# Optimization experiments

Hardware: AMD Instinct MI355X
Metric: run time of the kernel (lower is better)

The kernel has to match this reference:

```python
import jax, jax.numpy as jnp
import numpy as np

TEMPERATURE = 0.07
UNIFORMITY_THRESHOLD = 0.1
SEPARATION_MARGIN = 2.0
W_SUPCON = 1.0
W_SEPARATION = 0.5
W_UNIFORMITY = 0.5
NUM_MASKS = 6


def setup_inputs() -> dict:
    key = jax.random.key(0)
    k1, k2, k3 = jax.random.split(key, 3)
    B, H, Wd, D = 16, 33, 33, 512
    emb = jax.random.normal(k1, (B, H, Wd, D), dtype=jnp.float32)
    emb = emb / jnp.linalg.norm(emb, axis=-1, keepdims=True)  # module expects normalized embeddings
    masks = jax.random.uniform(k2, (B, NUM_MASKS, H, Wd), dtype=jnp.float32)
    is_forged = jax.random.uniform(k3, (B,), dtype=jnp.float32)
    return {"embeddings": emb, "masks": masks, "is_forged": is_forged}


def _labels(masks):
    # masks: (M, H, W). Channel i writes label i+1 where mask>0.5 (if channel has any mass);
    # later channels overwrite earlier -> equivalent to max over active hits.
    active = masks.sum(axis=(1, 2)) > 0  # (M,)
    hit = (masks > 0.5) & active[:, None, None]
    ids = jnp.arange(1, masks.shape[0] + 1)[:, None, None]
    return jnp.max(jnp.where(hit, ids, 0), axis=0).reshape(-1)  # (H*W,)


def _per_image(emb, masks, forged):
    H, W, D = emb.shape
    feat = emb.reshape(-1, D)  # (N, D)
    N = feat.shape[0]
    labels = _labels(masks)  # (N,) in 0..M
    L = masks.shape[0] + 1  # possible labels 0..6
    onehot = (labels[:, None] == jnp.arange(L)[None, :]).astype(feat.dtype)  # (N, L)
    cnt = onehot.sum(axis=0)  # (L,)
    sums = onehot.T @ feat  # (L, D) per-label sums
    mean_l = sums / jnp.maximum(cnt, 1.0)[:, None]  # safe per-label centroids

    # ---- SupCon (PixelSupConLoss) ----
    logits = (feat @ feat.T) / TEMPERATURE  # (N, N)
    logits = logits - jax.lax.stop_gradient(logits.max(axis=1, keepdims=True))
    same = (labels[:, None] == labels[None, :]).astype(feat.dtype)
    logits_mask = 1.0 - jnp.eye(N, dtype=feat.dtype)
    pos = same * logits_mask
    exp_l = jnp.exp(logits) * logits_mask
    log_prob = logits - jnp.log(exp_l.sum(axis=1, keepdims=True) + 1e-6)
    pos_sum = pos.sum(axis=1)
    mean_lp = (pos * log_prob).sum(axis=1) / jnp.where(pos_sum == 0, 1.0, pos_sum)
    anchor_valid = (pos_sum > 0).astype(feat.dtype)
    n_anchor = anchor_valid.sum()
    supcon = (-mean_lp * anchor_valid).sum() / jnp.maximum(n_anchor, 1.0)
    supcon_valid = n_anchor > 0

    # ---- Inter-instance separation ----
    present = cnt > 0
    cn = (mean_l ** 2).sum(axis=1)  # (L,)
    sq = cn[:, None] + cn[None, :] - 2.0 * (mean_l @ mean_l.T)  # squared centroid dists
    tri = jnp.triu(jnp.ones((L, L), dtype=bool), k=1)
    pair_valid = tri & present[:, None] & present[None, :]
    d = jnp.sqrt(jnp.where(pair_valid, jnp.maximum(sq, 0.0), 1.0))
    terms = jnp.where(pair_valid, jax.nn.relu(SEPARATION_MARGIN - d), 0.0)
    n_pairs = pair_valid.sum().astype(feat.dtype)
    sep = terms.sum() / jnp.maximum(n_pairs, 1.0)
    sep_valid = present.sum() >= 2

    # ---- Uniformity ----
    rn2 = (feat ** 2).sum(axis=1)  # (N,)
    q_l = onehot.T @ rn2  # (L,) per-label sum of squared norms
    var_l = q_l / jnp.maximum(cnt, 1.0) - (mean_l ** 2).sum(axis=1)  # E||e||^2 - ||mean||^2
    lbl_valid = (cnt >= 2) & (var_l > UNIFORMITY_THRESHOLD)
    inst_loss = jnp.where(lbl_valid, var_l - UNIFORMITY_THRESHOLD, 0.0).sum()
    n_lbl = lbl_valid.sum().astype(feat.dtype)
    uni_forged = inst_loss / jnp.maximum(n_lbl, 1.0)
    uni_forged_valid = n_lbl > 0
    mean_all = feat.mean(axis=0)
    var_all = ((feat - mean_all) ** 2).sum(axis=1).mean()
    uni_unf = jnp.where(var_all > UNIFORMITY_THRESHOLD, var_all - UNIFORMITY_THRESHOLD, 0.0)
    uni_unf_valid = var_all > UNIFORMITY_THRESHOLD

    is_f = forged >= 0.5
    uni = jnp.where(is_f, uni_forged, uni_unf)
    uni_valid = jnp.where(is_f, uni_forged_valid, uni_unf_valid)
    return supcon, supcon_valid, sep, sep_valid, uni, uni_valid


def _agg(vals, valids):
    v = valids.astype(vals.dtype)
    n = v.sum()
    return jnp.where(n > 0, (vals * v).sum() / jnp.maximum(n, 1.0), 0.0)


def reference(embeddings, masks, is_forged):
    sc, scv, sp, spv, un, unv = jax.vmap(_per_image)(embeddings, masks, is_forged)
    supcon = _agg(sc, scv)
    separation = _agg(sp, spv)
    uniformity = _agg(un, unv)
    return W_SUPCON * supcon + W_SEPARATION * separation + W_UNIFORMITY * uniformity
```

## Files before the change

### kernel.cpp

```cpp
#include <hip/hip_runtime.h>
#include <math.h>

#define NPIX 1089
#define DIM 512
#define NIMG 16
#define NLBL 8
#define NMASK 6
#define INVT 14.2857142857142857f

#define NGRP 72
#define NROWPAD 1152
#define NT9 9


typedef short v8s __attribute__((ext_vector_type(8)));
typedef float v4f __attribute__((ext_vector_type(4)));

__device__ __forceinline__ float wave_reduce(float x) {
#pragma unroll
  for (int o = 32; o > 0; o >>= 1) x += __shfl_xor(x, o, 64);
  return x;
}
__device__ __forceinline__ unsigned bfbits(float x) {
  unsigned u = __float_as_uint(x);
  return (u + 0x7FFFu + ((u >> 16) & 1u)) >> 16;
}
__device__ __forceinline__ unsigned pk(float lo, float hi) {
  return bfbits(lo) | (bfbits(hi) << 16);
}

__global__ __launch_bounds__(512) void k_packsum(const float* __restrict__ emb,
                                                 const float* __restrict__ masks,
                                                 uint2* __restrict__ bfemb2,
                                                 float* __restrict__ sums9,
                                                 unsigned* __restrict__ counter) {
  int b = blockIdx.y;
  int g9 = blockIdx.x >> 1, dh = blockIdx.x & 1;
  int tid = threadIdx.x, dd = tid & 63, w4 = tid >> 6, lane = tid & 63;
  __shared__ float msum[NMASK];
  __shared__ int slab[128];
  __shared__ float4 red[8 * 8 * 64];
  if (tid < NMASK) msum[tid] = 0.f;
  if (tid == 0 && blockIdx.x == 0 && b == 0) *counter = 0u;
  __syncthreads();
  {
    float am[NMASK] = {0.f, 0.f, 0.f, 0.f, 0.f, 0.f};
    for (int p = tid; p < NPIX; p += 512) {
#pragma unroll
      for (int c = 0; c < NMASK; c++) am[c] += masks[((size_t)b * NMASK + c) * NPIX + p];
    }
#pragma unroll
    for (int c = 0; c < NMASK; c++) {
      float v = wave_reduce(am[c]);
      if (lane == 0) atomicAdd(&msum[c], v);
    }
  }
  __syncthreads();
  if (tid < 128) {
    int r = g9 * 128 + tid;
    int lab = 7;
    if (r < NPIX) {
      lab = 0;
#pragma unroll
      for (int c = 0; c < NMASK; c++) {
        float mv = masks[((size_t)b * NMASK + c) * NPIX + r];
        if (mv > 0.5f && msum[c] > 0.f) lab = c + 1;
      }
    }
    slab[tid] = lab;
  }
  __syncthreads();
  float4 fa0 = {0,0,0,0}, fa1 = {0,0,0,0}, fa2 = {0,0,0,0}, fa3 = {0,0,0,0};
  float4 fa4 = {0,0,0,0}, fa5 = {0,0,0,0}, fa6 = {0,0,0,0}, fa7 = {0,0,0,0};
  int kc = dh * 8 + (dd >> 3), q = (dd >> 1) & 3, half = dd & 1;
#pragma unroll
  for (int k = 0; k < 16; k++) {
    int r = g9 * 128 + w4 + k * 8;
    bool v = r < NPIX;
    int rc = v ? r : (NPIX - 1);
    float4 x = ((const float4*)(emb + (size_t)(b * NPIX + rc) * DIM))[dh * 64 + dd];
    if (!v) x = make_float4(0.f, 0.f, 0.f, 0.f);
    uint2 o = make_uint2(pk(x.x, x.y), pk(x.z, x.w));
    bfemb2[((((size_t)(b * NGRP + (r >> 4)) * 16 + kc) * 64) + q * 16 + (r & 15)) * 2 + half] = o;
    int lab = __builtin_amdgcn_readfirstlane(slab[r - g9 * 128]);
    switch (lab) {
      case 0: fa0.x += x.x; fa0.y += x.y; fa0.z += x.z; fa0.w += x.w; break;
      case 1: fa1.x += x.x; fa1.y += x.y; fa1.z += x.z; fa1.w += x.w; break;
      case 2: fa2.x += x.x; fa2.y += x.y; fa2.z += x.z; fa2.w += x.w; break;
      case 3: fa3.x += x.x; fa3.y += x.y; fa3.z += x.z; fa3.w += x.w; break;
      case 4: fa4.x += x.x; fa4.y += x.y; fa4.z += x.z; fa4.w += x.w; break;
      case 5: fa5.x += x.x; fa5.y += x.y; fa5.z += x.z; fa5.w += x.w; break;
      case 6: fa6.x += x.x; fa6.y += x.y; fa6.z += x.z; fa6.w += x.w; break;
      default: fa7.x += x.x; fa7.y += x.y; fa7.z += x.z; fa7.w += x.w; break;
    }
  }
  red[(0 * 8 + w4) * 64 + dd] = fa0; red[(1 * 8 + w4) * 64 + dd] = fa1;
  red[(2 * 8 + w4) * 64 + dd] = fa2; red[(3 * 8 + w4) * 64 + dd] = fa3;
  red[(4 * 8 + w4) * 64 + dd] = fa4; red[(5 * 8 + w4) * 64 + dd] = fa5;
  red[(6 * 8 + w4) * 64 + dd] = fa6; red[(7 * 8 + w4) * 64 + dd] = fa7;
  __syncthreads();
  int l = tid >> 6, d2 = tid & 63;
  float4 s = {0,0,0,0};
#pragma unroll
  for (int ww = 0; ww < 8; ww++) {
    float4 t = red[(l * 8 + ww) * 64 + d2];
    s.x += t.x; s.y += t.y; s.z += t.z; s.w += t.w;
  }
  *(float4*)&sums9[(((size_t)(b * NT9 + g9) * NLBL + l) * DIM) + dh * 256 + d2 * 4] = s;
}

__global__ __launch_bounds__(256) void k_epass3(const uint4* __restrict__ bfemb4,
                                                float* __restrict__ E9) {
  int n = blockIdx.x;
  int img = ((n & 7) << 1) | ((n >> 3) & 1);
  int t = n >> 4;
  int it = 0, rem = t;
  while (rem >= NT9 - it) { rem -= NT9 - it; it++; }
  int jt = it + rem;
  int i0 = it * 128, j0 = jt * 128;
  bool diag = (it == jt);
  int tid = threadIdx.x, lane = tid & 63, w = tid >> 6;
  int wm = w >> 1, wn = w & 1;
  int quad = lane >> 4, l15 = lane & 15;
  __shared__ float Ered[2][128];
  __shared__ float Ecol[2][128];

  size_t uA[4], uB[4];
#pragma unroll
  for (int f = 0; f < 4; f++) {
    uA[f] = ((size_t)(img * NGRP + it * 8 + wm * 4 + f) * 16) * 64 + lane;
    uB[f] = ((size_t)(img * NGRP + jt * 8 + wn * 4 + f) * 16) * 64 + lane;
  }

  v4f acc[4][4];
#pragma unroll
  for (int mf = 0; mf < 4; mf++)
#pragma unroll
    for (int nf = 0; nf < 4; nf++) acc[mf][nf] = (v4f){0.f, 0.f, 0.f, 0.f};

  v8s a0[4], b0[4], a1[4], b1[4];
#define LOADG(kc, AR, BR)                                               \
  {                                                                     \
    _Pragma("unroll") for (int f = 0; f < 4; f++)                       \
        AR[f] = *(const v8s*)(bfemb4 + uA[f] + (kc) * 64);              \
    _Pragma("unroll") for (int f = 0; f < 4; f++)                       \
        BR[f] = *(const v8s*)(bfemb4 + uB[f] + (kc) * 64);              \
  }
#define MFMAG(AR, BR)                                                   \
  {                                                                     \
    _Pragma("unroll") for (int mf = 0; mf < 4; mf++)                    \
        _Pragma("unroll") for (int nf = 0; nf < 4; nf++)                \
            acc[mf][nf] = __builtin_amdgcn_mfma_f32_16x16x32_bf16(      \
                AR[mf], BR[nf], acc[mf][nf], 0, 0, 0);                  \
  }

  LOADG(0, a0, b0);
#pragma unroll
  for (int kc = 0; kc < 16; kc += 2) {
    if (kc + 1 < 16) LOADG(kc + 1, a1, b1);
    MFMAG(a0, b0);
    if (kc + 2 < 16) LOADG(kc + 2, a0, b0);
    MFMAG(a1, b1);
  }
#undef LOADG
#undef MFMAG

  float scol[4] = {0.f, 0.f, 0.f, 0.f};
#pragma unroll
  for (int mf = 0; mf < 4; mf++) {
#pragma unroll
    for (int rr = 0; rr < 4; rr++) {
      int i = i0 + wm * 64 + mf * 16 + quad * 4 + rr;
      float srow = 0.f;
#pragma unroll
      for (int nf = 0; nf < 4; nf++) {
        int j = j0 + wn * 64 + nf * 16 + l15;
        float e = __expf((acc[mf][nf][rr] - 1.f) * INVT);
        bool ok = (j < NPIX) && (!diag || (i != j && i < NPIX));
        e = ok ? e : 0.f;
        srow += e;
        scol[nf] += e;
      }
      srow += __shfl_xor(srow, 1); srow += __shfl_xor(srow, 2);
      srow += __shfl_xor(srow, 4); srow += __shfl_xor(srow, 8);
      if (l15 == 0) Ered[wn][wm * 64 + mf * 16 + quad * 4 + rr] = srow;
    }
  }
  if (!diag) {
#pragma unroll
    for (int nf = 0; nf < 4; nf++) {
      float s = scol[nf];
      s += __shfl_xor(s, 16); s += __shfl_xor(s, 32);
      if (quad == 0) Ecol[wm][wn * 64 + nf * 16 + l15] = s;
    }
  }
  __syncthreads();
  if (tid < 128) {
    E9[((size_t)img * NT9 + jt) * NROWPAD + i0 + tid] = Ered[0][tid] + Ered[1][tid];
    if (!diag)
      E9[((size_t)img * NT9 + it) * NROWPAD + j0 + tid] = Ecol[0][tid] + Ecol[1][tid];
  }
}

__global__ void k_imgfinal(const float* __restrict__ masks, const float* __restrict__ sums9,
                           const float* __restrict__ E9, const float* __restrict__ is_forged,
                           unsigned* __restrict__ counter, float* __restrict__ per_img,
                           float* __restrict__ out) {
  int b = blockIdx.x, tid = threadIdx.x;
  int wave = tid >> 6, lane = tid & 63;
  __shared__ float msum[NMASK];
  __shared__ int slab[NPIX];
  __shared__ float ssum[NLBL * DIM];
  __shared__ float sCnt[NLBL], sR[NLBL][NLBL];
  __shared__ float red4[4][NLBL];
  __shared__ float sLog, sNA;
  if (tid < NMASK) msum[tid] = 0.f;
  if (tid == 0) { sLog = 0.f; sNA = 0.f; }
  __syncthreads();
  {
    float am[NMASK] = {0.f, 0.f, 0.f, 0.f, 0.f, 0.f};
    for (int p = tid; p < NPIX; p += 256) {
#pragma unroll
      for (int c = 0; c < NMASK; c++) am[c] += masks[((size_t)b * NMASK + c) * NPIX + p];
    }
#pragma unroll
    for (int c = 0; c < NMASK; c++) {
      float v = wave_reduce(am[c]);
      if (lane == 0) atomicAdd(&msum[c], v);
    }
  }
  __syncthreads();
  {
    float c8[NLBL] = {0.f, 0.f, 0.f, 0.f, 0.f, 0.f, 0.f, 0.f};
    for (int p = tid; p < NPIX; p += 256) {
      int lab = 0;
#pragma unroll
      for (int c = 0; c < NMASK; c++) {
        float mv = masks[((size_t)b * NMASK + c) * NPIX + p];
        if (mv > 0.5f && msum[c] > 0.f) lab = c + 1;
      }
      slab[p] = lab;
#pragma unroll
      for (int l = 0; l < NLBL; l++) c8[l] += (lab == l) ? 1.f : 0.f;
    }
#pragma unroll
    for (int l = 0; l < NLBL; l++) c8[l] = wave_reduce(c8[l]);
    if (lane == 0) {
#pragma unroll
      for (int l = 0; l < NLBL; l++) red4[wave][l] = c8[l];
    }
  }
  __syncthreads();
  if (tid < NLBL)
    sCnt[tid] = red4[0][tid] + red4[1][tid] + red4[2][tid] + red4[3][tid];
  for (int o = tid; o < NLBL * DIM; o += 256) {
    float s = 0.f;
#pragma unroll
    for (int g = 0; g < NT9; g++) s += sums9[((size_t)(b * NT9 + g) * NLBL * DIM) + o];
    ssum[o] = s;
  }
  __syncthreads();
  float ll = 0.f, na = 0.f;
  for (int p = tid; p < NPIX; p += 256) {
    int lab = slab[p];
    if (sCnt[lab] >= 1.5f) {
      float e = 0.f;
#pragma unroll
      for (int s = 0; s < NT9; s++) e += E9[((size_t)b * NT9 + s) * NROWPAD + p];
      ll += logf(e + 1e-6f);
      na += 1.f;
    }
  }
  ll = wave_reduce(ll); na = wave_reduce(na);
  if (lane == 0) { atomicAdd(&sLog, ll); atomicAdd(&sNA, na); }
  for (int t = wave; t < 36; t += 4) {
    int a = 0, tt = t;
    while (tt >= NLBL - a) { tt -= NLBL - a; a++; }
    int bb = a + tt;
    float d0 = 0.f;
    for (int k = lane; k < DIM; k += 64) d0 += ssum[a * DIM + k] * ssum[bb * DIM + k];
    d0 = wave_reduce(d0);
    if (lane == 0) sR[a][bb] = d0;
  }
  __syncthreads();
  if (tid == 0) {
    float spos = 0.f;
    for (int l = 0; l < NLBL; l++) {
      float c = sCnt[l];
      if (c >= 1.5f) spos += (sR[l][l] - c) * INVT / (c - 1.f) - c * INVT;
    }
    float nA = sNA;
    float sc = nA > 0.f ? (sLog - spos) / nA : 0.f;
    float scv = nA > 0.f ? 1.f : 0.f;
    float inv[NLBL]; int present[NLBL]; int nPres = 0;
    for (int l = 0; l < NLBL; l++) {
      present[l] = sCnt[l] > 0.f;
      nPres += present[l];
      inv[l] = 1.f / fmaxf(sCnt[l], 1.f);
    }
    float sepsum = 0.f; int npairs = 0;
    for (int a = 0; a < NLBL; a++)
      for (int c = a + 1; c < NLBL; c++)
        if (present[a] && present[c]) {
          float sq_ = sR[a][a] * inv[a] * inv[a] + sR[c][c] * inv[c] * inv[c]
                    - 2.f * sR[a][c] * inv[a] * inv[c];
          float dd = sqrtf(fmaxf(sq_, 0.f));
          sepsum += fmaxf(2.f - dd, 0.f);
          npairs++;
        }
    float sep = npairs > 0 ? sepsum / (float)npairs : 0.f;
    float sepv = nPres >= 2 ? 1.f : 0.f;
    float inst = 0.f; int nlbl = 0;
    for (int l = 0; l < NLBL; l++) {
      float var = 1.f - sR[l][l] * inv[l] * inv[l];
      if (sCnt[l] >= 2.f && var > 0.1f) { inst += var - 0.1f; nlbl++; }
    }
    float unif = nlbl > 0 ? inst / (float)nlbl : 0.f;
    float unifv = nlbl > 0 ? 1.f : 0.f;
    float tot2 = 0.f;
    for (int a = 0; a < NLBL; a++) {
      tot2 += sR[a][a];
      for (int c = a + 1; c < NLBL; c++) tot2 += 2.f * sR[a][c];
    }
    float Nf = (float)NPIX;
    float var_all = 1.f - tot2 / (Nf * Nf);
    float uniu = var_all > 0.1f ? var_all - 0.1f : 0.f;
    float uniuv = var_all > 0.1f ? 1.f : 0.f;
    bool isf = is_forged[b] >= 0.5f;
    per_img[b * 6 + 0] = sc;
    per_img[b * 6 + 1] = scv;
    per_img[b * 6 + 2] = sep;
    per_img[b * 6 + 3] = sepv;
    per_img[b * 6 + 4] = isf ? unif : uniu;
    per_img[b * 6 + 5] = isf ? unifv : uniuv;
    __threadfence();
    unsigned tk = atomicAdd(counter, 1u);
    if (tk == NIMG - 1) {
      __threadfence();
      float accv[3] = {0.f, 0.f, 0.f}, accn[3] = {0.f, 0.f, 0.f};
      for (int bb = 0; bb < NIMG; bb++)
        for (int m = 0; m < 3; m++) {
          float v = per_img[bb * 6 + m * 2], val = per_img[bb * 6 + m * 2 + 1];
          accv[m] += v * val; accn[m] += val;
        }
      float scA = accn[0] > 0.f ? accv[0] / accn[0] : 0.f;
      float sepA = accn[1] > 0.f ? accv[1] / accn[1] : 0.f;
      float uniA = accn[2] > 0.f ? accv[2] / accn[2] : 0.f;
      out[0] = 1.0f * scA + 0.5f * sepA + 0.5f * uniA;
    }
  }
}

extern "C" void kernel_launch(void* const* d_in, const int* in_sizes, int n_in,
                              void* d_out, int out_size, void* d_ws, size_t ws_size,
                              hipStream_t stream) {
  const float* emb = (const float*)d_in[0];
  const float* masks = (const float*)d_in[1];
  const float* isf = (const float*)d_in[2];
  float* out = (float*)d_out;
  char* ws = (char*)d_ws;
  size_t off = 0;
  uint4* bfemb4 = (uint4*)(ws + off);
  off += (size_t)NIMG * NGRP * 16 * 64 * 16;
  float* E9 = (float*)(ws + off);     off += sizeof(float) * NIMG * NT9 * NROWPAD;
  float* sums9 = (float*)(ws + off);  off += sizeof(float) * NIMG * NT9 * NLBL * DIM;
  float* per_img = (float*)(ws + off); off += sizeof(float) * NIMG * 6;
  off = (off + 127) & ~(size_t)127;
  unsigned* counter = (unsigned*)(ws + off); off += 128;

  k_packsum<<<dim3(18, NIMG), 512, 0, stream>>>(emb, masks, (uint2*)bfemb4, sums9, counter);
  k_epass3<<<45 * NIMG, 256, 0, stream>>>(bfemb4, E9);
  k_imgfinal<<<NIMG, 256, 0, stream>>>(masks, sums9, E9, isf, counter, per_img, out);
}
```

Before: 142.7 us.

## Fuse per-image final reduction into GEMM kernel via last-block tail

Removes the separate per-image final kernel. The last of the 45 tile blocks for each image, detected with a per-image atomic counter, now does the final reduction itself. Labels and per-chunk label counts are precomputed in the pack kernel, so the tail no longer re-reads the masks or recomputes labels. This saves one kernel launch and its serialization gap. In exchange, the GEMM kernel carries roughly 18KB of extra shared memory for the tail, which may lower occupancy, and it switches log to the faster __logf.

Result: slower. 174.8 us (+22.5%).

```diff
diff --git a/kernel.cpp b/kernel.cpp
--- a/kernel.cpp
+++ b/kernel.cpp
@@ -33,15 +33,19 @@
                                                  const float* __restrict__ masks,
                                                  uint2* __restrict__ bfemb2,
                                                  float* __restrict__ sums9,
-                                                 unsigned* __restrict__ counter) {
+                                                 int* __restrict__ labels,
+                                                 float* __restrict__ cnt9,
+                                                 unsigned* __restrict__ counters) {
   int b = blockIdx.y;
   int g9 = blockIdx.x >> 1, dh = blockIdx.x & 1;
   int tid = threadIdx.x, dd = tid & 63, w4 = tid >> 6, lane = tid & 63;
   __shared__ float msum[NMASK];
   __shared__ int slab[128];
+  __shared__ int scnt[NLBL];
   __shared__ float4 red[8 * 8 * 64];
   if (tid < NMASK) msum[tid] = 0.f;
-  if (tid == 0 && blockIdx.x == 0 && b == 0) *counter = 0u;
+  if (tid < NLBL) scnt[tid] = 0;
+  if (b == 0 && blockIdx.x == 0 && tid < 17) counters[tid] = 0u;
   __syncthreads();
   {
     float am[NMASK] = {0.f, 0.f, 0.f, 0.f, 0.f, 0.f};
@@ -68,8 +72,13 @@
       }
     }
     slab[tid] = lab;
-  }
-  __syncthreads();
+    if (dh == 0) {
+      labels[b * NROWPAD + r] = lab;
+      if (r < NPIX) atomicAdd(&scnt[lab], 1);
+    }
+  }
+  __syncthreads();
+  if (dh == 0 && tid < NLBL) cnt9[((size_t)b * NT9 + g9) * NLBL + tid] = (float)scnt[tid];
   float4 fa0 = {0,0,0,0}, fa1 = {0,0,0,0}, fa2 = {0,0,0,0}, fa3 = {0,0,0,0};
   float4 fa4 = {0,0,0,0}, fa5 = {0,0,0,0}, fa6 = {0,0,0,0}, fa7 = {0,0,0,0};
   int kc = dh * 8 + (dd >> 3), q = (dd >> 1) & 3, half = dd & 1;
@@ -109,8 +118,15 @@
   *(float4*)&sums9[(((size_t)(b * NT9 + g9) * NLBL + l) * DIM) + dh * 256 + d2 * 4] = s;
 }
 
-__global__ __launch_bounds__(256) void k_epass3(const uint4* __restrict__ bfemb4,
-                                                float* __restrict__ E9) {
+__global__ __launch_bounds__(256) void k_epass4(const uint4* __restrict__ bfemb4,
+                                                const float* __restrict__ sums9,
+                                                const int* __restrict__ labels,
+                                                const float* __restrict__ cnt9,
+                                                const float* __restrict__ is_forged,
+                                                unsigned* __restrict__ counters,
+                                                float* __restrict__ E9,
+                                                float* __restrict__ per_img,
+                                                float* __restrict__ out) {
   int n = blockIdx.x;
   int img = ((n & 7) << 1) | ((n >> 3) & 1);
   int t = n >> 4;
@@ -124,6 +140,11 @@
   int quad = lane >> 4, l15 = lane & 15;
   __shared__ float Ered[2][128];
   __shared__ float Ecol[2][128];
+  __shared__ int slab[NPIX];
+  __shared__ float ssum[NLBL * DIM];
+  __shared__ float sCnt[NLBL], sR[NLBL][NLBL];
+  __shared__ float sLog, sNA;
+  __shared__ int isTail;
 
   size_t uA[4], uB[4];
 #pragma unroll
@@ -200,63 +221,25 @@
     if (!diag)
       E9[((size_t)img * NT9 + it) * NROWPAD + j0 + tid] = Ecol[0][tid] + Ecol[1][tid];
   }
-}
-
-__global__ void k_imgfinal(const float* __restrict__ masks, const float* __restrict__ sums9,
-                           const float* __restrict__ E9, const float* __restrict__ is_forged,
-                           unsigned* __restrict__ counter, float* __restrict__ per_img,
-                           float* __restrict__ out) {
-  int b = blockIdx.x, tid = threadIdx.x;
-  int wave = tid >> 6, lane = tid & 63;
-  __shared__ float msum[NMASK];
-  __shared__ int slab[NPIX];
-  __shared__ float ssum[NLBL * DIM];
-  __shared__ float sCnt[NLBL], sR[NLBL][NLBL];
-  __shared__ float red4[4][NLBL];
-  __shared__ float sLog, sNA;
-  if (tid < NMASK) msum[tid] = 0.f;
+  __threadfence();
+  __syncthreads();
+  if (tid == 0) isTail = (atomicAdd(&counters[img], 1u) == 44u);
+  __syncthreads();
+  if (!isTail) return;
+  __threadfence();
+
+  if (tid < NLBL) {
+    float s = 0.f;
+#pragma unroll
+    for (int g = 0; g < NT9; g++) s += cnt9[((size_t)img * NT9 + g) * NLBL + tid];
+    sCnt[tid] = s;
+  }
   if (tid == 0) { sLog = 0.f; sNA = 0.f; }
-  __syncthreads();
-  {
-    float am[NMASK] = {0.f, 0.f, 0.f, 0.f, 0.f, 0.f};
-    for (int p = tid; p < NPIX; p += 256) {
-#pragma unroll
-      for (int c = 0; c < NMASK; c++) am[c] += masks[((size_t)b * NMASK + c) * NPIX + p];
-    }
-#pragma unroll
-    for (int c = 0; c < NMASK; c++) {
-      float v = wave_reduce(am[c]);
-      if (lane == 0) atomicAdd(&msum[c], v);
-    }
-  }
-  __syncthreads();
-  {
-    float c8[NLBL] = {0.f, 0.f, 0.f, 0.f, 0.f, 0.f, 0.f, 0.f};
-    for (int p = tid; p < NPIX; p += 256) {
-      int lab = 0;
-#pragma unroll
-      for (int c = 0; c < NMASK; c++) {
-        float mv = masks[((size_t)b * NMASK + c) * NPIX + p];
-        if (mv > 0.5f && msum[c] > 0.f) lab = c + 1;
-      }
-      slab[p] = lab;
-#pragma unroll
-      for (int l = 0; l < NLBL; l++) c8[l] += (lab == l) ? 1.f : 0.f;
-    }
-#pragma unroll
-    for (int l = 0; l < NLBL; l++) c8[l] = wave_reduce(c8[l]);
-    if (lane == 0) {
-#pragma unroll
-      for (int l = 0; l < NLBL; l++) red4[wave][l] = c8[l];
-    }
-  }
-  __syncthreads();
-  if (tid < NLBL)
-    sCnt[tid] = red4[0][tid] + red4[1][tid] + red4[2][tid] + red4[3][tid];
+  for (int p = tid; p < NPIX; p += 256) slab[p] = labels[img * NROWPAD + p];
   for (int o = tid; o < NLBL * DIM; o += 256) {
     float s = 0.f;
 #pragma unroll
-    for (int g = 0; g < NT9; g++) s += sums9[((size_t)(b * NT9 + g) * NLBL * DIM) + o];
+    for (int g = 0; g < NT9; g++) s += sums9[((size_t)(img * NT9 + g) * NLBL * DIM) + o];
     ssum[o] = s;
   }
   __syncthreads();
@@ -266,15 +249,15 @@
     if (sCnt[lab] >= 1.5f) {
       float e = 0.f;
 #pragma unroll
-      for (int s = 0; s < NT9; s++) e += E9[((size_t)b * NT9 + s) * NROWPAD + p];
-      ll += logf(e + 1e-6f);
+      for (int s = 0; s < NT9; s++) e += E9[((size_t)img * NT9 + s) * NROWPAD + p];
+      ll += __logf(e + 1e-6f);
       na += 1.f;
     }
   }
   ll = wave_reduce(ll); na = wave_reduce(na);
   if (lane == 0) { atomicAdd(&sLog, ll); atomicAdd(&sNA, na); }
-  for (int t = wave; t < 36; t += 4) {
-    int a = 0, tt = t;
+  for (int tt0 = w; tt0 < 36; tt0 += 4) {
+    int a = 0, tt = tt0;
     while (tt >= NLBL - a) { tt -= NLBL - a; a++; }
     int bb = a + tt;
     float d0 = 0.f;
@@ -326,15 +309,15 @@
     float var_all = 1.f - tot2 / (Nf * Nf);
     float uniu = var_all > 0.1f ? var_all - 0.1f : 0.f;
     float uniuv = var_all > 0.1f ? 1.f : 0.f;
-    bool isf = is_forged[b] >= 0.5f;
-    per_img[b * 6 + 0] = sc;
-    per_img[b * 6 + 1] = scv;
-    per_img[b * 6 + 2] = sep;
-    per_img[b * 6 + 3] = sepv;
-    per_img[b * 6 + 4] = isf ? unif : uniu;
-    per_img[b * 6 + 5] = isf ? unifv : uniuv;
+    bool isf = is_forged[img] >= 0.5f;
+    per_img[img * 6 + 0] = sc;
+    per_img[img * 6 + 1] = scv;
+    per_img[img * 6 + 2] = sep;
+    per_img[img * 6 + 3] = sepv;
+    per_img[img * 6 + 4] = isf ? unif : uniu;
+    per_img[img * 6 + 5] = isf ? unifv : uniuv;
     __threadfence();
-    unsigned tk = atomicAdd(counter, 1u);
+    unsigned tk = atomicAdd(&counters[16], 1u);
     if (tk == NIMG - 1) {
       __threadfence();
       float accv[3] = {0.f, 0.f, 0.f}, accn[3] = {0.f, 0.f, 0.f};
@@ -364,11 +347,14 @@
   off += (size_t)NIMG * NGRP * 16 * 64 * 16;
   float* E9 = (float*)(ws + off);     off += sizeof(float) * NIMG * NT9 * NROWPAD;
   float* sums9 = (float*)(ws + off);  off += sizeof(float) * NIMG * NT9 * NLBL * DIM;
+  int* labels = (int*)(ws + off);     off += sizeof(int) * NIMG * NROWPAD;
+  float* cnt9 = (float*)(ws + off);   off += sizeof(float) * NIMG * NT9 * NLBL;
   float* per_img = (float*)(ws + off); off += sizeof(float) * NIMG * 6;
   off = (off + 127) & ~(size_t)127;
-  unsigned* counter = (unsigned*)(ws + off); off += 128;
-
-  k_packsum<<<dim3(18, NIMG), 512, 0, stream>>>(emb, masks, (uint2*)bfemb4, sums9, counter);
-  k_epass3<<<45 * NIMG, 256, 0, stream>>>(bfemb4, E9);
-  k_imgfinal<<<NIMG, 256, 0, stream>>>(masks, sums9, E9, isf, counter, per_img, out);
-}
+  unsigned* counters = (unsigned*)(ws + off); off += 128;
+
+  k_packsum<<<dim3(18, NIMG), 512, 0, stream>>>(emb, masks, (uint2*)bfemb4, sums9,
+                                                labels, cnt9, counters);
+  k_epass4<<<45 * NIMG, 256, 0, stream>>>(bfemb4, sums9, labels, cnt9, isf,
+                                          counters, E9, per_img, out);
+}
```
